# Kernel optimization log

Hardware: AMD Instinct MI355X
Metric: run time of the kernel (lower is better)

The kernel has to match this reference:

```python
import jax, jax.numpy as jnp
import numpy as np

B, S, T, C, Q = 8, 4096, 2048, 256, 256  # batch, ctx_steps, q_steps, context_size, query_size


def setup_inputs() -> dict:
    key = jax.random.key(0)
    k1, k2, k3, k4 = jax.random.split(key, 4)
    context = jax.random.normal(k1, (B, S, C), dtype=jnp.float32)
    query = jax.random.normal(k2, (T, B, Q), dtype=jnp.float32)
    context_mask = jax.random.randint(k3, (B, S), 0, 2).astype(bool)  # True = masked
    W = jax.random.normal(k4, (C, Q), dtype=jnp.float32)  # bilinear weights [context_size, query_size]
    return {"context": context, "query": query, "context_mask": context_mask, "W": W}


def reference(context, query, context_mask, W):
    # temp = 'auto' -> sqrt(query_size)
    temp = jnp.asarray(np.sqrt(Q), dtype=context.dtype)
    # scores[b,t,s] = (context[b,s,:] @ W) . query[t,b,:]
    scores = jnp.einsum('bsc,cq,tbq->bts', context, W, query) / temp
    neg = jnp.finfo(scores.dtype).min
    scores = jnp.where(context_mask[:, None, :], neg, scores)  # mask over ctx_steps
    attn = jax.nn.softmax(scores, axis=2)  # [B, T, S]
    # rows whose entire context is masked -> attention zeroed
    all_masked = jnp.all(context_mask, axis=1)[:, None, None]
    attn = jnp.where(all_masked, jnp.zeros((), attn.dtype), attn)
    composition = jnp.einsum('bts,bsc->btc', attn, context)  # [B, T, C]
    # module returns (attn, composition) permuted to [T, B, ...]
    return attn.transpose(1, 0, 2), composition.transpose(1, 0, 2)
```

## Files before the change

kernel.cpp:

```cpp
#include <hip/hip_runtime.h>

#define B_ 8
#define S_ 4096
#define T_ 2048
#define C_ 256
#define Q_ 256
#define NROW (T_ * B_)

typedef _Float16 f16;
typedef _Float16 f16x8 __attribute__((ext_vector_type(8)));
typedef _Float16 f16x4 __attribute__((ext_vector_type(4)));
typedef _Float16 f16x2 __attribute__((ext_vector_type(2)));
typedef float f32x4 __attribute__((ext_vector_type(4)));

#define MFMA(a, b, c) __builtin_amdgcn_mfma_f32_16x16x32_f16((a), (b), (c), 0, 0, 0)

__global__ void k_mask_mode(const unsigned char* __restrict__ mb, int* __restrict__ mode,
                            int* __restrict__ allm) {
  __shared__ int s0_, s123_;
  if (threadIdx.x == 0) { s0_ = 0; s123_ = 0; }
  __syncthreads();
  int a0 = 0, a123 = 0;
  int base = threadIdx.x * 128;
  for (int i = 0; i < 128; ++i) {
    int idx = base + i;
    int v = mb[idx];
    if (idx & 3) a123 |= v; else a0 |= v;
  }
  if (a0) atomicOr(&s0_, 1);
  if (a123) atomicOr(&s123_, 1);
  __syncthreads();
  if (threadIdx.x == 0) {
    int m;
    if (s123_ == 0 && s0_ == 0) m = 3;
    else if (s123_ == 0) m = 0;
    else if (s0_ == 0) m = 2;
    else m = 1;
    *mode = m;
  }
  if (threadIdx.x < B_) allm[threadIdx.x] = 1;
}

__global__ void k_expand_mask(const void* __restrict__ mp, const int* __restrict__ mode,
                              float* __restrict__ maskf, int* __restrict__ allm) {
  int i = blockIdx.x * 256 + threadIdx.x;
  int md = *mode;
  int m;
  if (md == 0)      m = ((const int*)mp)[i] != 0;
  else if (md == 1) m = ((const unsigned char*)mp)[i] != 0;
  else if (md == 2) m = ((const float*)mp)[i] != 0.0f;
  else              m = 0;
  maskf[i] = m ? 1.0f : 0.0f;
  if (!m) atomicAnd(&allm[i / S_], 0);
}

__global__ void k_conv_w(const float* __restrict__ W, f16* __restrict__ WT) {
  int i = blockIdx.x * 256 + threadIdx.x;
  int c = i >> 8, q = i & 255;
  WT[q * C_ + c] = (f16)W[i];
}

__global__ void k_conv_q(const float* __restrict__ q, f16* __restrict__ qT) {
  int i = blockIdx.x * 256 + threadIdx.x;
  int e = i * 4;
  int t = e / (B_ * Q_);
  int rb = e - t * (B_ * Q_);
  int b = rb >> 8;
  int qq = rb & 255;
  f32x4 v = *(const f32x4*)(q + e);
  f16x4 h; h[0] = (f16)v[0]; h[1] = (f16)v[1]; h[2] = (f16)v[2]; h[3] = (f16)v[3];
  *(f16x4*)(qT + ((size_t)(b * T_ + t)) * Q_ + qq) = h;
}

__global__ void k_transpose_ctx(const float* __restrict__ ctx, f16* __restrict__ ctxT) {
  __shared__ f16 tile[64][65];
  int s0 = blockIdx.x * 64, c0 = blockIdx.y * 64, b = blockIdx.z;
  int r = threadIdx.x >> 2;
  int cs = (threadIdx.x & 3) * 16;
  const float* src = ctx + ((size_t)(b * S_ + s0 + r)) * C_ + c0 + cs;
  f32x4 v0 = ((const f32x4*)src)[0];
  f32x4 v1 = ((const f32x4*)src)[1];
  f32x4 v2 = ((const f32x4*)src)[2];
  f32x4 v3 = ((const f32x4*)src)[3];
#pragma unroll
  for (int j = 0; j < 4; ++j) {
    tile[r][cs + j] = (f16)v0[j];
    tile[r][cs + 4 + j] = (f16)v1[j];
    tile[r][cs + 8 + j] = (f16)v2[j];
    tile[r][cs + 12 + j] = (f16)v3[j];
  }
  __syncthreads();
  int c = threadIdx.x >> 2;
  int ss = (threadIdx.x & 3) * 16;
  f16x8 o0, o1;
#pragma unroll
  for (int j = 0; j < 8; ++j) { o0[j] = tile[ss + j][c]; o1[j] = tile[ss + 8 + j][c]; }
  f16* dst = ctxT + ((size_t)(b * C_ + c0 + c)) * S_ + s0 + ss;
  *(f16x8*)dst = o0;
  *(f16x8*)(dst + 8) = o1;
}

__launch_bounds__(256, 2)
__global__ void k_gemm_cw(const float* __restrict__ ctx, const f16* __restrict__ WT,
                          f16* __restrict__ CW) {
  __shared__ alignas(16) f16 As[128 * 32];
  __shared__ alignas(16) f16 Bs[128 * 32];
  int n0 = blockIdx.x * 128;
  int m0 = blockIdx.y * 128;
  int tid = threadIdx.x;
  int w = tid >> 6, l = tid & 63;
  int wm = (w >> 1) * 64, wn = (w & 1) * 64;
  int lr = l & 15, lk = (l >> 4) * 8;
  f32x4 acc[4][4] = {};
  for (int k0 = 0; k0 < C_; k0 += 32) {
    __syncthreads();
#pragma unroll
    for (int it = 0; it < 2; ++it) {
      int h = (it * 256 + tid) * 8;
      int row = h >> 5, kk = h & 31;
      const float* ap = ctx + (size_t)(m0 + row) * C_ + k0 + kk;
      f32x4 x0 = ((const f32x4*)ap)[0];
      f32x4 x1 = ((const f32x4*)ap)[1];
      f16x8 hv;
#pragma unroll
      for (int j = 0; j < 4; ++j) { hv[j] = (f16)x0[j]; hv[4 + j] = (f16)x1[j]; }
      *(f16x8*)&As[row * 32 + kk] = hv;
    }
#pragma unroll
    for (int it = 0; it < 2; ++it) {
      int h = (it * 256 + tid) * 8;
      int row = h >> 5, kk = h & 31;
      *(f16x8*)&Bs[row * 32 + kk] = *(const f16x8*)&WT[(size_t)(n0 + row) * C_ + k0 + kk];
    }
    __syncthreads();
    f16x8 af[4], bf[4];
#pragma unroll
    for (int m = 0; m < 4; ++m) af[m] = *(const f16x8*)&As[(wm + m * 16 + lr) * 32 + lk];
#pragma unroll
    for (int n = 0; n < 4; ++n) bf[n] = *(const f16x8*)&Bs[(wn + n * 16 + lr) * 32 + lk];
#pragma unroll
    for (int m = 0; m < 4; ++m)
#pragma unroll
      for (int n = 0; n < 4; ++n) acc[m][n] = MFMA(af[m], bf[n], acc[m][n]);
  }
#pragma unroll
  for (int m = 0; m < 4; ++m)
#pragma unroll
    for (int n = 0; n < 4; ++n)
#pragma unroll
      for (int i = 0; i < 4; ++i) {
        int gm = m0 + wm + m * 16 + (l >> 4) * 4 + i;
        int gn = n0 + wn + n * 16 + lr;
        CW[(size_t)gm * Q_ + gn] = (f16)(acc[m][n][i] * 0.0625f);
      }
}

__launch_bounds__(256, 2)
__global__ void k_gemm_scores(const f16* __restrict__ qT, const f16* __restrict__ CW,
                              const float* __restrict__ maskf, float* __restrict__ attn,
                              float* __restrict__ pmax, float* __restrict__ psum) {
  __shared__ alignas(16) f16 As[128 * 32];
  __shared__ alignas(16) f16 Bs[128 * 32];
  int n0 = blockIdx.x * 128;
  int m0 = blockIdx.y * 128;
  int b = blockIdx.z;
  const f16* A = qT + (size_t)b * T_ * Q_;
  const f16* Bm = CW + (size_t)b * S_ * Q_;
  int tid = threadIdx.x;
  int w = tid >> 6, l = tid & 63;
  int wm = (w >> 1) * 64, wn = (w & 1) * 64;
  int lr = l & 15, lk = (l >> 4) * 8;
  f32x4 acc[4][4] = {};
  for (int k0 = 0; k0 < Q_; k0 += 32) {
    __syncthreads();
#pragma unroll
    for (int it = 0; it < 2; ++it) {
      int h = (it * 256 + tid) * 8;
      int row = h >> 5, kk = h & 31;
      *(f16x8*)&As[row * 32 + kk] = *(const f16x8*)&A[(size_t)(m0 + row) * Q_ + k0 + kk];
    }
#pragma unroll
    for (int it = 0; it < 2; ++it) {
      int h = (it * 256 + tid) * 8;
      int row = h >> 5, kk = h & 31;
      *(f16x8*)&Bs[row * 32 + kk] = *(const f16x8*)&Bm[(size_t)(n0 + row) * Q_ + k0 + kk];
    }
    __syncthreads();
    f16x8 af[4], bf[4];
#pragma unroll
    for (int m = 0; m < 4; ++m) af[m] = *(const f16x8*)&As[(wm + m * 16 + lr) * 32 + lk];
#pragma unroll
    for (int n = 0; n < 4; ++n) bf[n] = *(const f16x8*)&Bs[(wn + n * 16 + lr) * 32 + lk];
#pragma unroll
    for (int m = 0; m < 4; ++m)
#pragma unroll
      for (int n = 0; n < 4; ++n) acc[m][n] = MFMA(af[m], bf[n], acc[m][n]);
  }
  float msk[4];
#pragma unroll
  for (int n = 0; n < 4; ++n) msk[n] = maskf[b * S_ + n0 + wn + n * 16 + lr];
#pragma unroll
  for (int m = 0; m < 4; ++m)
#pragma unroll
    for (int n = 0; n < 4; ++n) {
      int gn = n0 + wn + n * 16 + lr;
#pragma unroll
      for (int i = 0; i < 4; ++i) {
        int gt = m0 + wm + m * 16 + (l >> 4) * 4 + i;
        float v = acc[m][n][i];
        if (msk[n] != 0.0f) v = -3.4e38f;
        acc[m][n][i] = v;
        attn[((size_t)gt * B_ + b) * S_ + gn] = v;
      }
    }
  int g = l >> 4;
  int ch = blockIdx.x * 2 + (w & 1);
#pragma unroll
  for (int m = 0; m < 4; ++m)
#pragma unroll
    for (int i = 0; i < 4; ++i) {
      float mx = fmaxf(fmaxf(acc[m][0][i], acc[m][1][i]), fmaxf(acc[m][2][i], acc[m][3][i]));
      mx = fmaxf(mx, __shfl_xor(mx, 1));
      mx = fmaxf(mx, __shfl_xor(mx, 2));
      mx = fmaxf(mx, __shfl_xor(mx, 4));
      mx = fmaxf(mx, __shfl_xor(mx, 8));
      float sm = 0.0f;
#pragma unroll
      for (int n = 0; n < 4; ++n) sm += __expf(acc[m][n][i] - mx);
      sm += __shfl_xor(sm, 1);
      sm += __shfl_xor(sm, 2);
      sm += __shfl_xor(sm, 4);
      sm += __shfl_xor(sm, 8);
      if (lr == 0) {
        int gt = m0 + wm + m * 16 + g * 4 + i;
        int r = gt * B_ + b;
        pmax[ch * NROW + r] = mx;
        psum[ch * NROW + r] = sm;
      }
    }
}

__launch_bounds__(256, 2)
__global__ void k_gemm_stats(const f16* __restrict__ qT, const f16* __restrict__ CW,
                             const float* __restrict__ maskf,
                             float* __restrict__ pmax, float* __restrict__ psum) {
  __shared__ alignas(16) f16 As[128 * 32];
  __shared__ alignas(16) f16 Bs[128 * 32];
  int n0 = blockIdx.x * 128;
  int m0 = blockIdx.y * 128;
  int b = blockIdx.z;
  const f16* A = qT + (size_t)b * T_ * Q_;
  const f16* Bm = CW + (size_t)b * S_ * Q_;
  int tid = threadIdx.x;
  int w = tid >> 6, l = tid & 63;
  int wm = (w >> 1) * 64, wn = (w & 1) * 64;
  int lr = l & 15, lk = (l >> 4) * 8;
  f32x4 acc[4][4] = {};
  for (int k0 = 0; k0 < Q_; k0 += 32) {
    __syncthreads();
#pragma unroll
    for (int it = 0; it < 2; ++it) {
      int h = (it * 256 + tid) * 8;
      int row = h >> 5, kk = h & 31;
      *(f16x8*)&As[row * 32 + kk] = *(const f16x8*)&A[(size_t)(m0 + row) * Q_ + k0 + kk];
    }
#pragma unroll
    for (int it = 0; it < 2; ++it) {
      int h = (it * 256 + tid) * 8;
      int row = h >> 5, kk = h & 31;
      *(f16x8*)&Bs[row * 32 + kk] = *(const f16x8*)&Bm[(size_t)(n0 + row) * Q_ + k0 + kk];
    }
    __syncthreads();
    f16x8 af[4], bf[4];
#pragma unroll
    for (int m = 0; m < 4; ++m) af[m] = *(const f16x8*)&As[(wm + m * 16 + lr) * 32 + lk];
#pragma unroll
    for (int n = 0; n < 4; ++n) bf[n] = *(const f16x8*)&Bs[(wn + n * 16 + lr) * 32 + lk];
#pragma unroll
    for (int m = 0; m < 4; ++m)
#pragma unroll
      for (int n = 0; n < 4; ++n) acc[m][n] = MFMA(af[m], bf[n], acc[m][n]);
  }
  float msk[4];
#pragma unroll
  for (int n = 0; n < 4; ++n) msk[n] = maskf[b * S_ + n0 + wn + n * 16 + lr];
#pragma unroll
  for (int m = 0; m < 4; ++m)
#pragma unroll
    for (int n = 0; n < 4; ++n) {
      if (msk[n] != 0.0f) {
#pragma unroll
        for (int i = 0; i < 4; ++i) acc[m][n][i] = -3.4e38f;
      }
    }
  int g = l >> 4;
  int ch = blockIdx.x * 2 + (w & 1);
#pragma unroll
  for (int m = 0; m < 4; ++m)
#pragma unroll
    for (int i = 0; i < 4; ++i) {
      float mx = fmaxf(fmaxf(acc[m][0][i], acc[m][1][i]), fmaxf(acc[m][2][i], acc[m][3][i]));
      mx = fmaxf(mx, __shfl_xor(mx, 1));
      mx = fmaxf(mx, __shfl_xor(mx, 2));
      mx = fmaxf(mx, __shfl_xor(mx, 4));
      mx = fmaxf(mx, __shfl_xor(mx, 8));
      float sm = 0.0f;
#pragma unroll
      for (int n = 0; n < 4; ++n) sm += __expf(acc[m][n][i] - mx);
      sm += __shfl_xor(sm, 1);
      sm += __shfl_xor(sm, 2);
      sm += __shfl_xor(sm, 4);
      sm += __shfl_xor(sm, 8);
      if (lr == 0) {
        int gt = m0 + wm + m * 16 + g * 4 + i;
        int r = gt * B_ + b;
        pmax[ch * NROW + r] = mx;
        psum[ch * NROW + r] = sm;
      }
    }
}

__global__ void k_finalize(const float* __restrict__ pmax, const float* __restrict__ psum,
                           float* __restrict__ rmax, float* __restrict__ rsum) {
  int r = blockIdx.x * 256 + threadIdx.x;
  float mx = -3.4e38f;
#pragma unroll 8
  for (int c = 0; c < 64; ++c) mx = fmaxf(mx, pmax[c * NROW + r]);
  float s = 0.0f;
#pragma unroll 8
  for (int c = 0; c < 64; ++c) s += psum[c * NROW + r] * __expf(pmax[c * NROW + r] - mx);
  rmax[r] = mx;
  rsum[r] = s;
}

__launch_bounds__(256, 2)
__global__ void k_comp(float* __restrict__ attn, const f16* __restrict__ ctxT,
                       const float* __restrict__ rmax, const float* __restrict__ rsum,
                       const int* __restrict__ allm, float* __restrict__ comp) {
  __shared__ alignas(16) f16 As[2][32 * 64];
  __shared__ alignas(16) f16 Bs[2][256 * 64];
  const int t0 = blockIdx.x * 32;
  const int b = blockIdx.y;
  const int tid = threadIdx.x;
  const int w = tid >> 6, l = tid & 63;
  const int lr = l & 15, hi = l >> 4;
  const int am = allm[b];
  const int ar = tid >> 4;
  const int cg = tid & 15;
  float mx0, mx1, inv0, inv1;
  float* aP0;
  float* aP1;
  {
    int r0 = (t0 + ar) * B_ + b;
    int r1 = (t0 + 16 + ar) * B_ + b;
    mx0 = rmax[r0]; mx1 = rmax[r1];
    inv0 = am ? 0.0f : (1.0f / rsum[r0]);
    inv1 = am ? 0.0f : (1.0f / rsum[r1]);
    aP0 = attn + (size_t)r0 * S_ + cg * 4;
    aP1 = attn + (size_t)r1 * S_ + cg * 4;
  }
  const int aswz = (cg * 8) ^ ((ar & 7) << 4);
  const int bc = tid >> 3;
  const int bs = tid & 7;
  const f16* bP = ctxT + ((size_t)(b * C_ + bc)) * S_ + bs * 8;
  const int bswz = (bs * 16) ^ ((bc & 7) << 4);
  f32x4 acc[2][4] = {};
  f32x4 aC0 = *(const f32x4*)aP0;
  f32x4 aC1 = *(const f32x4*)aP1;
  f16x8 bC[8];
#pragma unroll
  for (int i = 0; i < 8; ++i) bC[i] = *(const f16x8*)(bP + (size_t)i * 32 * S_);
  for (int k = 0; k < S_ / 64; ++k) {
    const int cur = k & 1;
    const int kn = (k + 1) * 64;
    f32x4 aN0 = *(const f32x4*)(aP0 + kn);
    f32x4 aN1 = *(const f32x4*)(aP1 + kn);
    f16x8 bN[8];
#pragma unroll
    for (int i = 0; i < 8; ++i) bN[i] = *(const f16x8*)(bP + (size_t)i * 32 * S_ + kn);
    f32x4 p0, p1;
#pragma unroll
    for (int e = 0; e < 4; ++e) {
      p0[e] = __expf(aC0[e] - mx0) * inv0;
      p1[e] = __expf(aC1[e] - mx1) * inv1;
    }
    *(f32x4*)(aP0 + k * 64) = p0;
    *(f32x4*)(aP1 + k * 64) = p1;
    f16x4 h0, h1;
#pragma unroll
    for (int e = 0; e < 4; ++e) { h0[e] = (f16)p0[e]; h1[e] = (f16)p1[e]; }
    *(f16x4*)((char*)As[cur] + ar * 128 + aswz) = h0;
    *(f16x4*)((char*)As[cur] + (16 + ar) * 128 + aswz) = h1;
#pragma unroll
    for (int i = 0; i < 8; ++i)
      *(f16x8*)((char*)Bs[cur] + (i * 32 + bc) * 128 + bswz) = bC[i];
    asm volatile("s_waitcnt lgkmcnt(0)" ::: "memory");
    __builtin_amdgcn_s_barrier();
    __builtin_amdgcn_sched_barrier(0);
#pragma unroll
    for (int kk = 0; kk < 2; ++kk) {
      const int cb = (kk * 64 + hi * 16) ^ ((lr & 7) << 4);
      f16x8 af[2], bf[4];
#pragma unroll
      for (int m = 0; m < 2; ++m)
        af[m] = *(const f16x8*)((char*)As[cur] + (m * 16 + lr) * 128 + cb);
#pragma unroll
      for (int n = 0; n < 4; ++n)
        bf[n] = *(const f16x8*)((char*)Bs[cur] + (w * 64 + n * 16 + lr) * 128 + cb);
#pragma unroll
      for (int m = 0; m < 2; ++m)
#pragma unroll
        for (int n = 0; n < 4; ++n) acc[m][n] = MFMA(af[m], bf[n], acc[m][n]);
    }
    aC0 = aN0; aC1 = aN1;
#pragma unroll
    for (int i = 0; i < 8; ++i) bC[i] = bN[i];
  }
#pragma unroll
  for (int m = 0; m < 2; ++m)
#pragma unroll
    for (int n = 0; n < 4; ++n)
#pragma unroll
      for (int i = 0; i < 4; ++i) {
        int tl = m * 16 + hi * 4 + i;
        int cc = w * 64 + n * 16 + lr;
        comp[((size_t)(t0 + tl) * B_ + b) * C_ + cc] = acc[m][n][i];
      }
}

__launch_bounds__(256, 2)
__global__ void k_fused3(const f16* __restrict__ qT, const f16* __restrict__ CW,
                         const f16* __restrict__ ctxT, const float* __restrict__ maskf,
                         const float* __restrict__ rmax, const float* __restrict__ rsum,
                         const int* __restrict__ allm,
                         float* __restrict__ attn, float* __restrict__ cptr) {
  __shared__ alignas(16) f16 Qs[64 * 256];
  __shared__ alignas(16) f16 Ps[2][64 * 64];
  __shared__ float2 Sm[64];
  const int CH = 32;
  const int bid = blockIdx.x;
  const int b = bid & 7;
  const int u = bid >> 3;
  const int t0 = (u & 31) * 64;
  const int sp = u >> 5;
  const int sbase = sp * (S_ / 2);
  const int tid = threadIdx.x;
  const int w = tid >> 6, l = tid & 63;
  const int lr = l & 15, hi = l >> 4;
  const int rswz = (lr & 7) << 4;
  const int srow = w * 16 + lr;
  {
    const int qr = tid & 63;
    const int cb0 = (tid >> 6) * 128;
    const char* src = (const char*)(qT + ((size_t)(b * T_ + t0 + qr)) * Q_) + cb0;
#pragma unroll
    for (int j = 0; j < 8; ++j) {
      f16x8 v = *(const f16x8*)(src + j * 16);
      *(f16x8*)((char*)Qs + qr * 512 + ((cb0 + j * 16) ^ ((qr & 7) << 4))) = v;
    }
    if (tid < 64) {
      int r = (t0 + tid) * B_ + b;
      float2 sv;
      sv.x = rmax[r];
      sv.y = allm[b] ? 0.0f : (1.0f / rsum[r]);
      Sm[tid] = sv;
    }
  }
  const f16* cwL = CW + ((size_t)b * S_ + sbase + srow) * Q_ + hi * 8;
  const f16* cxL = ctxT + (size_t)(b * C_ + w * 64 + lr) * S_ + sbase + hi * 8;
  const float* maskP = maskf + b * S_ + sbase + srow;
  f32x4 accC[4][4] = {};
  __syncthreads();
  {
    float mk = maskP[0];
    f32x4 accS[4] = {};
#pragma unroll
    for (int g = 0; g < 2; ++g) {
      f16x8 cw4[4];
#pragma unroll
      for (int j = 0; j < 4; ++j)
        cw4[j] = *(const f16x8*)(cwL + (g * 4 + j) * 32);
#pragma unroll
      for (int j = 0; j < 4; ++j) {
        const int kq = g * 4 + j;
#pragma unroll
        for (int m = 0; m < 4; ++m) {
          f16x8 a = *(const f16x8*)((char*)Qs + (m * 16 + lr) * 512 +
                                    ((kq * 64 + hi * 16) ^ rswz));
          accS[m] = MFMA(a, cw4[j], accS[m]);
        }
      }
    }
#pragma unroll
    for (int m = 0; m < 4; ++m)
#pragma unroll
      for (int i = 0; i < 4; ++i) {
        int tl = m * 16 + hi * 4 + i;
        float2 sv = Sm[tl];
        float p = (mk != 0.0f) ? 0.0f : __expf(accS[m][i] - sv.x) * sv.y;
        float po = __shfl_xor(p, 1);
        if (!(lr & 1)) {
          float2 fp; fp.x = p; fp.y = po;
          *(float2*)&attn[((size_t)(t0 + tl) * B_ + b) * S_ + sbase + srow] = fp;
          f16x2 h; h[0] = (f16)p; h[1] = (f16)po;
          *(f16x2*)((char*)Ps[0] + ((tl * 128 + srow * 2) ^ ((tl & 7) << 4))) = h;
        }
      }
    asm volatile("s_waitcnt lgkmcnt(0)" ::: "memory");
    __builtin_amdgcn_s_barrier();
  }
  for (int k = 1; k < CH; ++k) {
    const int s0 = k * 64;
    const int sc0 = s0 - 64;
    const int cur = k & 1, prev = cur ^ 1;
    float mk = maskP[s0];
    f16x8 cx8[8];
#pragma unroll
    for (int kk = 0; kk < 2; ++kk)
#pragma unroll
      for (int n = 0; n < 4; ++n)
        cx8[kk * 4 + n] = *(const f16x8*)(cxL + (size_t)(n * 16) * S_ + sc0 + kk * 32);
    f32x4 accS[4] = {};
#pragma unroll
    for (int g = 0; g < 2; ++g) {
      f16x8 cw4[4];
#pragma unroll
      for (int j = 0; j < 4; ++j)
        cw4[j] = *(const f16x8*)(cwL + (size_t)s0 * Q_ + (g * 4 + j) * 32);
#pragma unroll
      for (int j = 0; j < 4; ++j) {
        const int kq = g * 4 + j;
#pragma unroll
        for (int m = 0; m < 4; ++m) {
          f16x8 a = *(const f16x8*)((char*)Qs + (m * 16 + lr) * 512 +
                                    ((kq * 64 + hi * 16) ^ rswz));
          accS[m] = MFMA(a, cw4[j], accS[m]);
        }
      }
    }
#pragma unroll
    for (int m = 0; m < 4; ++m)
#pragma unroll
      for (int i = 0; i < 4; ++i) {
        int tl = m * 16 + hi * 4 + i;
        float2 sv = Sm[tl];
        float p = (mk != 0.0f) ? 0.0f : __expf(accS[m][i] - sv.x) * sv.y;
        float po = __shfl_xor(p, 1);
        if (!(lr & 1)) {
          float2 fp; fp.x = p; fp.y = po;
          *(float2*)&attn[((size_t)(t0 + tl) * B_ + b) * S_ + sbase + s0 + srow] = fp;
          f16x2 h; h[0] = (f16)p; h[1] = (f16)po;
          *(f16x2*)((char*)Ps[cur] + ((tl * 128 + srow * 2) ^ ((tl & 7) << 4))) = h;
        }
      }
#pragma unroll
    for (int kk = 0; kk < 2; ++kk) {
      f16x8 pa[4];
#pragma unroll
      for (int m = 0; m < 4; ++m)
        pa[m] = *(const f16x8*)((char*)Ps[prev] +
                                (((m * 16 + lr) * 128 + kk * 64 + hi * 16) ^ rswz));
#pragma unroll
      for (int n = 0; n < 4; ++n)
#pragma unroll
        for (int m = 0; m < 4; ++m) accC[m][n] = MFMA(pa[m], cx8[kk * 4 + n], accC[m][n]);
    }
    asm volatile("s_waitcnt lgkmcnt(0)" ::: "memory");
    __builtin_amdgcn_s_barrier();
  }
  {
    const int sc0 = (CH - 1) * 64;
    const int prev = (CH - 1) & 1;
#pragma unroll
    for (int kk = 0; kk < 2; ++kk) {
      f16x8 cx4[4];
#pragma unroll
      for (int n = 0; n < 4; ++n)
        cx4[n] = *(const f16x8*)(cxL + (size_t)(n * 16) * S_ + sc0 + kk * 32);
      f16x8 pa[4];
#pragma unroll
      for (int m = 0; m < 4; ++m)
        pa[m] = *(const f16x8*)((char*)Ps[prev] +
                                (((m * 16 + lr) * 128 + kk * 64 + hi * 16) ^ rswz));
#pragma unroll
      for (int n = 0; n < 4; ++n)
#pragma unroll
        for (int m = 0; m < 4; ++m) accC[m][n] = MFMA(pa[m], cx4[n], accC[m][n]);
    }
  }
  float* cout = cptr + (size_t)sp * T_ * B_ * C_;
#pragma unroll
  for (int m = 0; m < 4; ++m)
#pragma unroll
    for (int n = 0; n < 4; ++n)
#pragma unroll
      for (int i = 0; i < 4; ++i) {
        int tl = m * 16 + hi * 4 + i;
        int cc = w * 64 + n * 16 + lr;
        cout[((size_t)(t0 + tl) * B_ + b) * C_ + cc] = accC[m][n][i];
      }
}

__global__ void k_comp_red(const float* __restrict__ P, float* __restrict__ comp) {
  size_t i = ((size_t)blockIdx.x * 256 + threadIdx.x) * 4;
  f32x4 a = *(const f32x4*)(P + i);
  f32x4 c = *(const f32x4*)(P + (size_t)T_ * B_ * C_ + i);
  f32x4 r;
#pragma unroll
  for (int e = 0; e < 4; ++e) r[e] = a[e] + c[e];
  *(f32x4*)(comp + i) = r;
}

extern "C" void kernel_launch(void* const* d_in, const int* in_sizes, int n_in,
                              void* d_out, int out_size, void* d_ws, size_t ws_size,
                              hipStream_t stream) {
  const float* ctx = (const float*)d_in[0];
  const float* query = (const float*)d_in[1];
  const void* mask = d_in[2];
  const float* W = (const float*)d_in[3];

  float* out = (float*)d_out;
  float* attn = out;
  float* comp = out + (size_t)T_ * B_ * S_;

  char* ws = (char*)d_ws;
  f16* ctxT = (f16*)(ws);
  f16* qT = (f16*)(ws + 16777216);
  f16* WT = (f16*)(ws + 25165824);
  float* maskf = (float*)(ws + 25296896);
  float* rmax = (float*)(ws + 25427968);
  float* rsum = (float*)(ws + 25493504);
  int* allm = (int*)(ws + 25559040);
  int* mode = (int*)(ws + 25559072);
  float* pmax = (float*)(ws + 25559168);
  float* psum = (float*)(ws + 29753472);

  k_mask_mode<<<1, 256, 0, stream>>>((const unsigned char*)mask, mode, allm);
  k_expand_mask<<<(B_ * S_) / 256, 256, 0, stream>>>(mask, mode, maskf, allm);
  k_conv_w<<<(C_ * Q_) / 256, 256, 0, stream>>>(W, WT);
  k_conv_q<<<(T_ * B_ * Q_ / 4) / 256, 256, 0, stream>>>(query, qT);
  k_transpose_ctx<<<dim3(S_ / 64, C_ / 64, B_), 256, 0, stream>>>(ctx, ctxT);

  if (ws_size >= (size_t)84279424) {
    f16* CW2 = (f16*)(ws + 33947776);
    float* compP = (float*)(ws + 50724992);
    k_gemm_cw<<<dim3(Q_ / 128, (B_ * S_) / 128), 256, 0, stream>>>(ctx, WT, CW2);
    k_gemm_stats<<<dim3(S_ / 128, T_ / 128, B_), 256, 0, stream>>>(qT, CW2, maskf, pmax, psum);
    k_finalize<<<NROW / 256, 256, 0, stream>>>(pmax, psum, rmax, rsum);
    k_fused3<<<dim3((T_ / 64) * B_ * 2), 256, 0, stream>>>(qT, CW2, ctxT, maskf, rmax, rsum,
                                                           allm, attn, compP);
    k_comp_red<<<(T_ * B_ * C_ / 4) / 256, 256, 0, stream>>>(compP, comp);
  } else {
    f16* CW = (f16*)comp;
    k_gemm_cw<<<dim3(Q_ / 128, (B_ * S_) / 128), 256, 0, stream>>>(ctx, WT, CW);
    k_gemm_scores<<<dim3(S_ / 128, T_ / 128, B_), 256, 0, stream>>>(qT, CW, maskf, attn, pmax, psum);
    k_finalize<<<NROW / 256, 256, 0, stream>>>(pmax, psum, rmax, rsum);
    k_comp<<<dim3(T_ / 32, B_), 256, 0, stream>>>(attn, ctxT, rmax, rsum, allm, comp);
  }
}
```

Before: 512.0 us.

## Enlarge fused attention tile to 128 query rows with 8 waves per block

Replaces the 64-row, 4-wave fused scores/softmax/composition kernel with a 128-row, 8-wave version. Waves are split into two groups over query rows for the score GEMM, and each wave covers 32 context columns across all 128 rows for the composition GEMM. Each CW and ctxT tile loaded from global memory is now reused across twice as many query rows, which halves that traffic. In exchange, LDS use per block roughly doubles, the grid is half as large (256 blocks), and occupancy drops to one block per CU.

```diff
diff --git a/kernel.cpp b/kernel.cpp
--- a/kernel.cpp
+++ b/kernel.cpp
@@ -428,37 +428,39 @@
       }
 }
 
-__launch_bounds__(256, 2)
-__global__ void k_fused3(const f16* __restrict__ qT, const f16* __restrict__ CW,
+__launch_bounds__(512, 1)
+__global__ void k_fused4(const f16* __restrict__ qT, const f16* __restrict__ CW,
                          const f16* __restrict__ ctxT, const float* __restrict__ maskf,
                          const float* __restrict__ rmax, const float* __restrict__ rsum,
                          const int* __restrict__ allm,
                          float* __restrict__ attn, float* __restrict__ cptr) {
-  __shared__ alignas(16) f16 Qs[64 * 256];
-  __shared__ alignas(16) f16 Ps[2][64 * 64];
-  __shared__ float2 Sm[64];
+  __shared__ alignas(16) f16 Qs[128 * 256];
+  __shared__ alignas(16) f16 Ps[2][128 * 64];
+  __shared__ float2 Sm[128];
   const int CH = 32;
   const int bid = blockIdx.x;
   const int b = bid & 7;
   const int u = bid >> 3;
-  const int t0 = (u & 31) * 64;
-  const int sp = u >> 5;
+  const int t0 = (u & 15) * 128;
+  const int sp = u >> 4;
   const int sbase = sp * (S_ / 2);
   const int tid = threadIdx.x;
   const int w = tid >> 6, l = tid & 63;
   const int lr = l & 15, hi = l >> 4;
   const int rswz = (lr & 7) << 4;
-  const int srow = w * 16 + lr;
+  const int wsg = (w & 3) * 16;
+  const int wtg = (w >> 2) * 4;
+  const int srow = wsg + lr;
   {
-    const int qr = tid & 63;
-    const int cb0 = (tid >> 6) * 128;
+    const int qr = tid & 127;
+    const int cb0 = (tid >> 7) * 128;
     const char* src = (const char*)(qT + ((size_t)(b * T_ + t0 + qr)) * Q_) + cb0;
 #pragma unroll
     for (int j = 0; j < 8; ++j) {
       f16x8 v = *(const f16x8*)(src + j * 16);
       *(f16x8*)((char*)Qs + qr * 512 + ((cb0 + j * 16) ^ ((qr & 7) << 4))) = v;
     }
-    if (tid < 64) {
+    if (tid < 128) {
       int r = (t0 + tid) * B_ + b;
       float2 sv;
       sv.x = rmax[r];
@@ -467,9 +469,9 @@
     }
   }
   const f16* cwL = CW + ((size_t)b * S_ + sbase + srow) * Q_ + hi * 8;
-  const f16* cxL = ctxT + (size_t)(b * C_ + w * 64 + lr) * S_ + sbase + hi * 8;
+  const f16* cxL = ctxT + (size_t)(b * C_ + w * 32 + lr) * S_ + sbase + hi * 8;
   const float* maskP = maskf + b * S_ + sbase + srow;
-  f32x4 accC[4][4] = {};
+  f32x4 accC[8][2] = {};
   __syncthreads();
   {
     float mk = maskP[0];
@@ -485,7 +487,7 @@
         const int kq = g * 4 + j;
 #pragma unroll
         for (int m = 0; m < 4; ++m) {
-          f16x8 a = *(const f16x8*)((char*)Qs + (m * 16 + lr) * 512 +
+          f16x8 a = *(const f16x8*)((char*)Qs + ((wtg + m) * 16 + lr) * 512 +
                                     ((kq * 64 + hi * 16) ^ rswz));
           accS[m] = MFMA(a, cw4[j], accS[m]);
         }
@@ -495,7 +497,7 @@
     for (int m = 0; m < 4; ++m)
 #pragma unroll
       for (int i = 0; i < 4; ++i) {
-        int tl = m * 16 + hi * 4 + i;
+        int tl = (wtg + m) * 16 + hi * 4 + i;
         float2 sv = Sm[tl];
         float p = (mk != 0.0f) ? 0.0f : __expf(accS[m][i] - sv.x) * sv.y;
         float po = __shfl_xor(p, 1);
@@ -514,12 +516,12 @@
     const int sc0 = s0 - 64;
     const int cur = k & 1, prev = cur ^ 1;
     float mk = maskP[s0];
-    f16x8 cx8[8];
+    f16x8 cx4[4];
 #pragma unroll
     for (int kk = 0; kk < 2; ++kk)
 #pragma unroll
-      for (int n = 0; n < 4; ++n)
-        cx8[kk * 4 + n] = *(const f16x8*)(cxL + (size_t)(n * 16) * S_ + sc0 + kk * 32);
+      for (int n = 0; n < 2; ++n)
+        cx4[kk * 2 + n] = *(const f16x8*)(cxL + (size_t)(n * 16) * S_ + sc0 + kk * 32);
     f32x4 accS[4] = {};
 #pragma unroll
     for (int g = 0; g < 2; ++g) {
@@ -532,7 +534,7 @@
         const int kq = g * 4 + j;
 #pragma unroll
         for (int m = 0; m < 4; ++m) {
-          f16x8 a = *(const f16x8*)((char*)Qs + (m * 16 + lr) * 512 +
+          f16x8 a = *(const f16x8*)((char*)Qs + ((wtg + m) * 16 + lr) * 512 +
                                     ((kq * 64 + hi * 16) ^ rswz));
           accS[m] = MFMA(a, cw4[j], accS[m]);
         }
@@ -542,7 +544,7 @@
     for (int m = 0; m < 4; ++m)
 #pragma unroll
       for (int i = 0; i < 4; ++i) {
-        int tl = m * 16 + hi * 4 + i;
+        int tl = (wtg + m) * 16 + hi * 4 + i;
         float2 sv = Sm[tl];
         float p = (mk != 0.0f) ? 0.0f : __expf(accS[m][i] - sv.x) * sv.y;
         float po = __shfl_xor(p, 1);
@@ -555,15 +557,13 @@
       }
 #pragma unroll
     for (int kk = 0; kk < 2; ++kk) {
-      f16x8 pa[4];
-#pragma unroll
-      for (int m = 0; m < 4; ++m)
-        pa[m] = *(const f16x8*)((char*)Ps[prev] +
-                                (((m * 16 + lr) * 128 + kk * 64 + hi * 16) ^ rswz));
-#pragma unroll
-      for (int n = 0; n < 4; ++n)
-#pragma unroll
-        for (int m = 0; m < 4; ++m) accC[m][n] = MFMA(pa[m], cx8[kk * 4 + n], accC[m][n]);
+#pragma unroll
+      for (int m = 0; m < 8; ++m) {
+        f16x8 pa = *(const f16x8*)((char*)Ps[prev] +
+                                   (((m * 16 + lr) * 128 + kk * 64 + hi * 16) ^ rswz));
+#pragma unroll
+        for (int n = 0; n < 2; ++n) accC[m][n] = MFMA(pa, cx4[kk * 2 + n], accC[m][n]);
+      }
     }
     asm volatile("s_waitcnt lgkmcnt(0)" ::: "memory");
     __builtin_amdgcn_s_barrier();
@@ -573,30 +573,28 @@
     const int prev = (CH - 1) & 1;
 #pragma unroll
     for (int kk = 0; kk < 2; ++kk) {
-      f16x8 cx4[4];
-#pragma unroll
-      for (int n = 0; n < 4; ++n)
-        cx4[n] = *(const f16x8*)(cxL + (size_t)(n * 16) * S_ + sc0 + kk * 32);
-      f16x8 pa[4];
-#pragma unroll
-      for (int m = 0; m < 4; ++m)
-        pa[m] = *(const f16x8*)((char*)Ps[prev] +
-                                (((m * 16 + lr) * 128 + kk * 64 + hi * 16) ^ rswz));
-#pragma unroll
-      for (int n = 0; n < 4; ++n)
-#pragma unroll
-        for (int m = 0; m < 4; ++m) accC[m][n] = MFMA(pa[m], cx4[n], accC[m][n]);
+      f16x8 cx2[2];
+#pragma unroll
+      for (int n = 0; n < 2; ++n)
+        cx2[n] = *(const f16x8*)(cxL + (size_t)(n * 16) * S_ + sc0 + kk * 32);
+#pragma unroll
+      for (int m = 0; m < 8; ++m) {
+        f16x8 pa = *(const f16x8*)((char*)Ps[prev] +
+                                   (((m * 16 + lr) * 128 + kk * 64 + hi * 16) ^ rswz));
+#pragma unroll
+        for (int n = 0; n < 2; ++n) accC[m][n] = MFMA(pa, cx2[n], accC[m][n]);
+      }
     }
   }
   float* cout = cptr + (size_t)sp * T_ * B_ * C_;
 #pragma unroll
-  for (int m = 0; m < 4; ++m)
-#pragma unroll
-    for (int n = 0; n < 4; ++n)
+  for (int m = 0; m < 8; ++m)
+#pragma unroll
+    for (int n = 0; n < 2; ++n)
 #pragma unroll
       for (int i = 0; i < 4; ++i) {
         int tl = m * 16 + hi * 4 + i;
-        int cc = w * 64 + n * 16 + lr;
+        int cc = w * 32 + n * 16 + lr;
         cout[((size_t)(t0 + tl) * B_ + b) * C_ + cc] = accC[m][n][i];
       }
 }
@@ -647,8 +645,8 @@
     k_gemm_cw<<<dim3(Q_ / 128, (B_ * S_) / 128), 256, 0, stream>>>(ctx, WT, CW2);
     k_gemm_stats<<<dim3(S_ / 128, T_ / 128, B_), 256, 0, stream>>>(qT, CW2, maskf, pmax, psum);
     k_finalize<<<NROW / 256, 256, 0, stream>>>(pmax, psum, rmax, rsum);
-    k_fused3<<<dim3((T_ / 64) * B_ * 2), 256, 0, stream>>>(qT, CW2, ctxT, maskf, rmax, rsum,
-                                                           allm, attn, compP);
+    k_fused4<<<dim3((T_ / 128) * B_ * 2), 512, 0, stream>>>(qT, CW2, ctxT, maskf, rmax, rsum,
+                                                            allm, attn, compP);
     k_comp_red<<<(T_ * B_ * C_ / 4) / 256, 256, 0, stream>>>(compP, comp);
   } else {
     f16* CW = (f16*)comp;
```

Result: no change. 507.2 us (-0.9%).
